# Performance work log

Measured on AMD Instinct MI355X. Metric: run time of the kernel, lower is better.

Reference implementation:

```python
import jax, jax.numpy as jnp
import numpy as np


def setup_inputs() -> dict:
    key = jax.random.key(0)
    k1, k2, k3, k4, k5 = jax.random.split(key, 5)
    N, T, D, H = 256, 64, 1024, 1024
    x = jax.random.normal(k1, (N, T, D), dtype=jnp.float32)
    A = jax.random.normal(k2, (N, H, 4, 4), dtype=jnp.float32)
    Wx = jax.random.normal(k3, (D, 4 * H), dtype=jnp.float32) / np.sqrt(D)
    Wh = jax.random.normal(k4, (H, 4 * H), dtype=jnp.float32) / np.sqrt(H)
    Wattn = jax.random.normal(k5, (H, 4 * H), dtype=jnp.float32) / np.sqrt(H)
    b = jnp.zeros((4 * H,), dtype=jnp.float32)
    return {"x": x, "A": A, "Wx": Wx, "Wh": Wh, "Wattn": Wattn, "b": b}


def reference(x, A, Wx, Wh, Wattn, b):
    N, T, D = x.shape
    H = A.shape[1]
    A_flat = A.reshape(N, H, 16)           # (N, H, 16) flattened 4x4 grid
    scale = 1.0 / jnp.sqrt(jnp.asarray(H, dtype=x.dtype))

    h0 = A.mean(axis=(2, 3))               # (N, H)
    c0 = h0

    def step(carry, xt):
        prev_h, prev_c = carry
        # scaled dot-product attention over the 16 spatial locations
        scores = jnp.einsum('nh,nhl->nl', prev_h, A_flat) * scale  # (N, 16)
        w = jax.nn.softmax(scores, axis=1)
        attn = jnp.einsum('nhl,nl->nh', A_flat, w)                 # (N, H)
        # fused LSTM gate pre-activation
        a = xt @ Wx + prev_h @ Wh + attn @ Wattn + b               # (N, 4H)
        ai, af, ao, ag = jnp.split(a, 4, axis=1)
        i = jax.nn.sigmoid(ai)
        f = jax.nn.sigmoid(af)
        o = jax.nn.sigmoid(ao)
        g = jnp.tanh(ag)
        next_c = f * prev_c + i * g
        next_h = o * jnp.tanh(next_c)
        return (next_h, next_c), next_h

    xs = jnp.swapaxes(x, 0, 1)             # (T, N, D)
    _, hs = jax.lax.scan(step, (h0, c0), xs)
    return jnp.swapaxes(hs, 0, 1)          # (N, T, H)
```

## Files before the change

kernel.cpp:

```cpp
#include <hip/hip_runtime.h>

typedef _Float16 f16;
typedef _Float16 f16x4 __attribute__((ext_vector_type(4)));
typedef _Float16 f16x8 __attribute__((ext_vector_type(8)));
typedef float f32x4 __attribute__((ext_vector_type(4)));

#define N_ 256
#define T_ 64
#define D_ 1024
#define H_ 1024
#define K3 3072
#define G4 4096

__global__ void k_transpose(const float* __restrict__ Wx, const float* __restrict__ Wh,
                            const float* __restrict__ Wattn, f16* __restrict__ W3T) {
    __shared__ float tile[32][33];
    int j0 = blockIdx.x * 32;
    int k0 = blockIdx.y * 32;
    int tx = threadIdx.x;
    int ty = threadIdx.y;
    for (int i = 0; i < 4; i++) {
        int k = k0 + ty + i * 8;
        const float* W = (k < 1024) ? Wx : ((k < 2048) ? Wh : Wattn);
        int kr = k & 1023;
        tile[ty + i * 8][tx] = W[(size_t)kr * 4096 + j0 + tx];
    }
    __syncthreads();
    for (int i = 0; i < 4; i++) {
        int j = j0 + ty + i * 8;
        W3T[(size_t)j * K3 + k0 + tx] = (f16)tile[tx][ty + i * 8];
    }
}

__global__ void k_castA(const float* __restrict__ A, f16* __restrict__ A16) {
    int i = blockIdx.x * 256 + threadIdx.x;
    float4 v = ((const float4*)A)[i];
    f16x4 h4 = {(f16)v.x, (f16)v.y, (f16)v.z, (f16)v.w};
    ((f16x4*)A16)[i] = h4;
}

__global__ void k_castX(const float* __restrict__ x, f16* __restrict__ x16) {
    size_t i = (size_t)blockIdx.x * 2048 + (size_t)threadIdx.x * 8;
    float4 v0 = *(const float4*)(x + i);
    float4 v1 = *(const float4*)(x + i + 4);
    f16x8 h;
    h[0] = (f16)v0.x; h[1] = (f16)v0.y; h[2] = (f16)v0.z; h[3] = (f16)v0.w;
    h[4] = (f16)v1.x; h[5] = (f16)v1.y; h[6] = (f16)v1.z; h[7] = (f16)v1.w;
    *(f16x8*)(x16 + i) = h;
}

__global__ void k_init(const float* __restrict__ A, f16* __restrict__ Zh,
                       float* __restrict__ c, float* __restrict__ spart) {
    int n = blockIdx.x;
    int tid = threadIdx.x;
    __shared__ float sred[256][16];
    float s[16];
#pragma unroll
    for (int l = 0; l < 16; l++) s[l] = 0.f;
    for (int i = 0; i < 4; i++) {
        int h = tid + i * 256;
        const float* Ap = A + (size_t)n * 16384 + h * 16;
        float a[16];
        float sum = 0.f;
#pragma unroll
        for (int l = 0; l < 16; l++) { a[l] = Ap[l]; sum += a[l]; }
        float h0 = sum * (1.f / 16.f);
        c[n * 1024 + h] = h0;
        Zh[n * 1024 + h] = (f16)h0;
#pragma unroll
        for (int l = 0; l < 16; l++) s[l] += h0 * a[l];
    }
#pragma unroll
    for (int l = 0; l < 16; l++) sred[tid][l] = s[l];
    __syncthreads();
    for (int st = 128; st > 0; st >>= 1) {
        if (tid < st) {
#pragma unroll
            for (int l = 0; l < 16; l++) sred[tid][l] += sred[tid + st][l];
        }
        __syncthreads();
    }
    if (tid < 16) spart[(size_t)n * 16 + tid] = sred[0][tid];
    for (int i = 0; i < 4; i++) {
        int idx = tid * 4 + i;
        if (idx < 1008) {
            int ht = 1 + (idx >> 4);
            int l = idx & 15;
            spart[((size_t)ht * 256 + n) * 16 + l] = 0.f;
        }
    }
}

__global__ void k_attn(const float* __restrict__ spart, const f16* __restrict__ A16,
                       f16* __restrict__ Za) {
    int n = blockIdx.x;
    int tid = threadIdx.x;
    __shared__ float sred[16][17];
    __shared__ float sfin[16];
    int g = tid >> 4;
    int l = tid & 15;
    float p = 0.f;
#pragma unroll
    for (int i = 0; i < 4; i++) {
        int ht = g + i * 16;
        p += spart[((size_t)ht * 256 + n) * 16 + l];
    }
    sred[g][l] = p;
    __syncthreads();
    if (tid < 16) {
        float s = 0.f;
#pragma unroll
        for (int gg = 0; gg < 16; gg++) s += sred[gg][tid];
        sfin[tid] = s;
    }
    __syncthreads();
    float w[16];
    float mx = -1e30f;
#pragma unroll
    for (int ll = 0; ll < 16; ll++) { w[ll] = sfin[ll] * 0.03125f; mx = fmaxf(mx, w[ll]); }
    float sum = 0.f;
#pragma unroll
    for (int ll = 0; ll < 16; ll++) { w[ll] = __expf(w[ll] - mx); sum += w[ll]; }
    float inv = 1.f / sum;
#pragma unroll
    for (int ll = 0; ll < 16; ll++) w[ll] *= inv;
    for (int i = 0; i < 4; i++) {
        int h = tid * 4 + i;
        const f16* Ap = A16 + (size_t)n * 16384 + h * 16;
        f16x8 a0 = *(const f16x8*)(Ap);
        f16x8 a1 = *(const f16x8*)(Ap + 8);
        float acc = 0.f;
#pragma unroll
        for (int ll = 0; ll < 8; ll++) acc += (float)a0[ll] * w[ll] + (float)a1[ll] * w[ll + 8];
        Za[n * 1024 + h] = (f16)acc;
    }
}

__global__ __launch_bounds__(512, 2) void k_step(
    const f16* __restrict__ x16, const f16* __restrict__ W3T,
    const f16* __restrict__ Zin, f16* __restrict__ Zout,
    const f16* __restrict__ Za, const f16* __restrict__ A16,
    const float* __restrict__ b, float* __restrict__ c,
    float* __restrict__ spart, float* __restrict__ out, int t) {
    __shared__ float Gs[4][4][64 * 17];
    __shared__ float Hs[64 * 17];

    int tid = threadIdx.x;
    int wave = tid >> 6;
    int lane = tid & 63;
    int m16 = lane & 15;
    int quad = lane >> 4;
    int bid = blockIdx.x;
    int ht = bid & 63;
    int n0 = (bid >> 6) << 6;
    int hc = ht * 16;

    f32x4 acc[4][4];
#pragma unroll
    for (int g = 0; g < 4; g++)
#pragma unroll
        for (int m = 0; m < 4; m++) acc[g][m] = (f32x4){0.f, 0.f, 0.f, 0.f};

    const f16* brow[4];
#pragma unroll
    for (int g = 0; g < 4; g++)
        brow[g] = W3T + (size_t)(g * 1024 + hc + m16) * K3 + quad * 8;

    size_t offx[4], offz[4];
#pragma unroll
    for (int mt = 0; mt < 4; mt++) {
        int n = n0 + mt * 16 + m16;
        offx[mt] = (size_t)n * (T_ * 1024);
        offz[mt] = (size_t)n * 1024;
    }
    const f16* xbase = x16 + (size_t)t * 1024 + quad * 8;
    const f16* zbase0 = Zin + quad * 8;
    const f16* zbase1 = Za + quad * 8;

    int kbase = wave * 384;
#pragma unroll 2
    for (int s = 0; s < 12; s++) {
        int k = kbase + s * 32;
        int seg = k >> 10;
        int kk = k & 1023;
        const f16* base;
        const size_t* off;
        if (seg == 0)      { base = xbase;  off = offx; }
        else if (seg == 1) { base = zbase0; off = offz; }
        else               { base = zbase1; off = offz; }
        f16x8 a[4], bb[4];
#pragma unroll
        for (int mt = 0; mt < 4; mt++) a[mt] = *(const f16x8*)(base + off[mt] + kk);
#pragma unroll
        for (int g = 0; g < 4; g++) bb[g] = *(const f16x8*)(brow[g] + k);
#pragma unroll
        for (int g = 0; g < 4; g++)
#pragma unroll
            for (int mt = 0; mt < 4; mt++)
                acc[g][mt] = __builtin_amdgcn_mfma_f32_16x16x32_f16(a[mt], bb[g], acc[g][mt], 0, 0, 0);
    }

    if (wave < 4) {
#pragma unroll
        for (int g = 0; g < 4; g++)
#pragma unroll
            for (int mt = 0; mt < 4; mt++)
#pragma unroll
                for (int r = 0; r < 4; r++)
                    Gs[wave][g][(mt * 16 + quad * 4 + r) * 17 + m16] = acc[g][mt][r];
    }
    __syncthreads();
    if (wave >= 4) {
        int sl = wave - 4;
#pragma unroll
        for (int g = 0; g < 4; g++)
#pragma unroll
            for (int mt = 0; mt < 4; mt++)
#pragma unroll
                for (int r = 0; r < 4; r++)
                    Gs[sl][g][(mt * 16 + quad * 4 + r) * 17 + m16] += acc[g][mt][r];
    }
    __syncthreads();

    for (int i = 0; i < 2; i++) {
        int idx = i * 512 + tid;
        int nn = idx >> 4;
        int hh = idx & 15;
        int gi = nn * 17 + hh;
        int gn = n0 + nn;
        int gh = hc + hh;
        float ai = Gs[0][0][gi] + Gs[1][0][gi] + Gs[2][0][gi] + Gs[3][0][gi] + b[gh];
        float af = Gs[0][1][gi] + Gs[1][1][gi] + Gs[2][1][gi] + Gs[3][1][gi] + b[1024 + gh];
        float ao = Gs[0][2][gi] + Gs[1][2][gi] + Gs[2][2][gi] + Gs[3][2][gi] + b[2048 + gh];
        float ag = Gs[0][3][gi] + Gs[1][3][gi] + Gs[2][3][gi] + Gs[3][3][gi] + b[3072 + gh];
        float ig = 1.f / (1.f + __expf(-ai));
        float fg = 1.f / (1.f + __expf(-af));
        float og = 1.f / (1.f + __expf(-ao));
        float gg = tanhf(ag);
        float cn = fg * c[gn * 1024 + gh] + ig * gg;
        c[gn * 1024 + gh] = cn;
        float hn = og * tanhf(cn);
        out[((size_t)gn * T_ + t) * 1024 + gh] = hn;
        Zout[gn * 1024 + gh] = (f16)hn;
        Hs[gi] = hn;
    }
    __syncthreads();

    for (int i = 0; i < 2; i++) {
        int idx = i * 512 + tid;
        int nn = idx >> 4;
        int l = idx & 15;
        int gn = n0 + nn;
        const f16* Ap = A16 + (size_t)gn * 16384 + hc * 16 + l;
        float s = 0.f;
#pragma unroll
        for (int hh = 0; hh < 16; hh++)
            s += Hs[nn * 17 + hh] * (float)Ap[hh * 16];
        spart[((size_t)ht * 256 + gn) * 16 + l] = s;
    }
}

extern "C" void kernel_launch(void* const* d_in, const int* in_sizes, int n_in,
                              void* d_out, int out_size, void* d_ws, size_t ws_size,
                              hipStream_t stream) {
    const float* x     = (const float*)d_in[0];
    const float* A     = (const float*)d_in[1];
    const float* Wx    = (const float*)d_in[2];
    const float* Wh    = (const float*)d_in[3];
    const float* Wattn = (const float*)d_in[4];
    const float* b     = (const float*)d_in[5];
    float* out = (float*)d_out;

    char* ws = (char*)d_ws;
    size_t off = 0;
    f16* W3T = (f16*)(ws + off); off += (size_t)G4 * K3 * 2;
    f16* x16 = (f16*)(ws + off); off += (size_t)N_ * T_ * D_ * 2;
    f16* A16 = (f16*)(ws + off); off += (size_t)N_ * H_ * 16 * 2;
    f16* Zh0 = (f16*)(ws + off); off += (size_t)N_ * H_ * 2;
    f16* Zh1 = (f16*)(ws + off); off += (size_t)N_ * H_ * 2;
    f16* Za  = (f16*)(ws + off); off += (size_t)N_ * H_ * 2;
    float* c = (float*)(ws + off); off += (size_t)N_ * H_ * 4;
    float* spart = (float*)(ws + off); off += (size_t)64 * N_ * 16 * 4;

    k_transpose<<<dim3(128, 96), dim3(32, 8), 0, stream>>>(Wx, Wh, Wattn, W3T);
    k_castA<<<4096, 256, 0, stream>>>(A, A16);
    k_castX<<<8192, 256, 0, stream>>>(x, x16);
    k_init<<<256, 256, 0, stream>>>(A, Zh0, c, spart);
    for (int t = 0; t < T_; t++) {
        f16* Zin  = (t & 1) ? Zh1 : Zh0;
        f16* Zout = (t & 1) ? Zh0 : Zh1;
        k_attn<<<256, 256, 0, stream>>>(spart, A16, Za);
        k_step<<<256, 512, 0, stream>>>(x16, W3T, Zin, Zout, Za, A16, b, c, spart, out, t);
    }
}
```

Baseline: 2.240 ms.

## Pack weights, inputs, hidden state and A into MFMA-tile-contiguous layouts

Weights are transposed into per-(h-tile, gate, k-slice) blocks of 16x32 halves, and x, h and the attention context are stored as [k-slice][n][32]. This lets each wave's MFMA operand loads hit contiguous 512-byte chunks instead of strided rows. A is transposed to [n][l][h] so the attention and score kernels use vectorized f16x8 loads, and the h16 write is vectorized. Launch bounds are raised to request 4 blocks per CU, which may increase register pressure or spilling.

```diff
diff --git a/kernel.cpp b/kernel.cpp
--- a/kernel.cpp
+++ b/kernel.cpp
@@ -13,7 +13,7 @@
 #define G4 4096
 
 __global__ void k_transpose(const float* __restrict__ Wx, const float* __restrict__ Wh,
-                            const float* __restrict__ Wattn, f16* __restrict__ W3T) {
+                            const float* __restrict__ Wattn, f16* __restrict__ W3P) {
     __shared__ float tile[32][33];
     int j0 = blockIdx.x * 32;
     int k0 = blockIdx.y * 32;
@@ -28,28 +28,52 @@
     __syncthreads();
     for (int i = 0; i < 4; i++) {
         int j = j0 + ty + i * 8;
-        W3T[(size_t)j * K3 + k0 + tx] = (f16)tile[tx][ty + i * 8];
-    }
-}
-
-__global__ void k_castA(const float* __restrict__ A, f16* __restrict__ A16) {
-    int i = blockIdx.x * 256 + threadIdx.x;
-    float4 v = ((const float4*)A)[i];
-    f16x4 h4 = {(f16)v.x, (f16)v.y, (f16)v.z, (f16)v.w};
-    ((f16x4*)A16)[i] = h4;
-}
-
-__global__ void k_castX(const float* __restrict__ x, f16* __restrict__ x16) {
-    size_t i = (size_t)blockIdx.x * 2048 + (size_t)threadIdx.x * 8;
-    float4 v0 = *(const float4*)(x + i);
-    float4 v1 = *(const float4*)(x + i + 4);
+        int ht = (j & 1023) >> 4;
+        int g = j >> 10;
+        int m16 = j & 15;
+        W3P[(size_t)((ht * 4 + g) * 96 + blockIdx.y) * 512 + m16 * 32 + tx] =
+            (f16)tile[tx][ty + i * 8];
+    }
+}
+
+__global__ void k_packX(const float* __restrict__ x, f16* __restrict__ xp) {
+    int bid = blockIdx.x;
+    int n = bid >> 6;
+    int t = bid & 63;
+    int k = threadIdx.x * 8;
+    const float* src = x + ((size_t)(n * 64 + t)) * 1024 + k;
+    float4 v0 = *(const float4*)src;
+    float4 v1 = *(const float4*)(src + 4);
     f16x8 h;
     h[0] = (f16)v0.x; h[1] = (f16)v0.y; h[2] = (f16)v0.z; h[3] = (f16)v0.w;
     h[4] = (f16)v1.x; h[5] = (f16)v1.y; h[6] = (f16)v1.z; h[7] = (f16)v1.w;
-    *(f16x8*)(x16 + i) = h;
-}
-
-__global__ void k_init(const float* __restrict__ A, f16* __restrict__ Zh,
+    int s = k >> 5, o = k & 31;
+    *(f16x8*)(xp + ((size_t)(t * 32 + s) * 256 + n) * 32 + o) = h;
+}
+
+__global__ void k_packA(const float* __restrict__ A, f16* __restrict__ A16T) {
+    __shared__ f16 tile[256][17];
+    int n = blockIdx.x;
+    int tid = threadIdx.x;
+    for (int c4 = 0; c4 < 4; c4++) {
+        int h = c4 * 256 + tid;
+        const float* Ap = A + (size_t)n * 16384 + h * 16;
+#pragma unroll
+        for (int l = 0; l < 16; l++) tile[tid][l] = (f16)Ap[l];
+        __syncthreads();
+        int l = tid >> 4;
+        int hs = (tid & 15) * 16;
+        f16 v[16];
+#pragma unroll
+        for (int j = 0; j < 16; j++) v[j] = tile[hs + j][l];
+        f16* dst = A16T + (size_t)n * 16384 + l * 1024 + c4 * 256 + hs;
+        *(f16x8*)dst = *(f16x8*)v;
+        *(f16x8*)(dst + 8) = *(f16x8*)(v + 8);
+        __syncthreads();
+    }
+}
+
+__global__ void k_init(const float* __restrict__ A, f16* __restrict__ zp0,
                        float* __restrict__ c, float* __restrict__ spart) {
     int n = blockIdx.x;
     int tid = threadIdx.x;
@@ -66,7 +90,7 @@
         for (int l = 0; l < 16; l++) { a[l] = Ap[l]; sum += a[l]; }
         float h0 = sum * (1.f / 16.f);
         c[n * 1024 + h] = h0;
-        Zh[n * 1024 + h] = (f16)h0;
+        zp0[((size_t)(h >> 5) * 256 + n) * 32 + (h & 31)] = (f16)h0;
 #pragma unroll
         for (int l = 0; l < 16; l++) s[l] += h0 * a[l];
     }
@@ -91,8 +115,8 @@
     }
 }
 
-__global__ void k_attn(const float* __restrict__ spart, const f16* __restrict__ A16,
-                       f16* __restrict__ Za) {
+__global__ void k_attn(const float* __restrict__ spart, const f16* __restrict__ A16T,
+                       f16* __restrict__ zap) {
     int n = blockIdx.x;
     int tid = threadIdx.x;
     __shared__ float sred[16][17];
@@ -101,10 +125,8 @@
     int l = tid & 15;
     float p = 0.f;
 #pragma unroll
-    for (int i = 0; i < 4; i++) {
-        int ht = g + i * 16;
-        p += spart[((size_t)ht * 256 + n) * 16 + l];
-    }
+    for (int i = 0; i < 4; i++)
+        p += spart[((size_t)(g + i * 16) * 256 + n) * 16 + l];
     sred[g][l] = p;
     __syncthreads();
     if (tid < 16) {
@@ -124,22 +146,28 @@
     float inv = 1.f / sum;
 #pragma unroll
     for (int ll = 0; ll < 16; ll++) w[ll] *= inv;
-    for (int i = 0; i < 4; i++) {
-        int h = tid * 4 + i;
-        const f16* Ap = A16 + (size_t)n * 16384 + h * 16;
-        f16x8 a0 = *(const f16x8*)(Ap);
-        f16x8 a1 = *(const f16x8*)(Ap + 8);
-        float acc = 0.f;
-#pragma unroll
-        for (int ll = 0; ll < 8; ll++) acc += (float)a0[ll] * w[ll] + (float)a1[ll] * w[ll + 8];
-        Za[n * 1024 + h] = (f16)acc;
-    }
-}
-
-__global__ __launch_bounds__(512, 2) void k_step(
-    const f16* __restrict__ x16, const f16* __restrict__ W3T,
-    const f16* __restrict__ Zin, f16* __restrict__ Zout,
-    const f16* __restrict__ Za, const f16* __restrict__ A16,
+    if (tid < 128) {
+        int h = tid * 8;
+        float acc[8];
+#pragma unroll
+        for (int e = 0; e < 8; e++) acc[e] = 0.f;
+#pragma unroll
+        for (int ll = 0; ll < 16; ll++) {
+            f16x8 av = *(const f16x8*)(A16T + (size_t)n * 16384 + ll * 1024 + h);
+#pragma unroll
+            for (int e = 0; e < 8; e++) acc[e] += (float)av[e] * w[ll];
+        }
+        f16x8 hv;
+#pragma unroll
+        for (int e = 0; e < 8; e++) hv[e] = (f16)acc[e];
+        *(f16x8*)(zap + ((size_t)(h >> 5) * 256 + n) * 32 + (h & 31)) = hv;
+    }
+}
+
+__global__ __launch_bounds__(512, 4) void k_step(
+    const f16* __restrict__ xp, const f16* __restrict__ W3P,
+    const f16* __restrict__ zin, f16* __restrict__ zout,
+    const f16* __restrict__ zap, const f16* __restrict__ A16T,
     const float* __restrict__ b, float* __restrict__ c,
     float* __restrict__ spart, float* __restrict__ out, int t) {
     __shared__ float Gs[4][4][64 * 17];
@@ -164,35 +192,27 @@
     const f16* brow[4];
 #pragma unroll
     for (int g = 0; g < 4; g++)
-        brow[g] = W3T + (size_t)(g * 1024 + hc + m16) * K3 + quad * 8;
-
-    size_t offx[4], offz[4];
-#pragma unroll
-    for (int mt = 0; mt < 4; mt++) {
-        int n = n0 + mt * 16 + m16;
-        offx[mt] = (size_t)n * (T_ * 1024);
-        offz[mt] = (size_t)n * 1024;
-    }
-    const f16* xbase = x16 + (size_t)t * 1024 + quad * 8;
-    const f16* zbase0 = Zin + quad * 8;
-    const f16* zbase1 = Za + quad * 8;
-
-    int kbase = wave * 384;
+        brow[g] = W3P + (size_t)((ht * 4 + g) * 96) * 512 + m16 * 32 + quad * 8;
+
+    size_t offm[4];
+#pragma unroll
+    for (int mt = 0; mt < 4; mt++)
+        offm[mt] = (size_t)(n0 + mt * 16 + m16) * 32 + quad * 8;
+    const f16* bx = xp + (size_t)t * 262144;
+
+    int sg0 = wave * 12;
 #pragma unroll 2
     for (int s = 0; s < 12; s++) {
-        int k = kbase + s * 32;
-        int seg = k >> 10;
-        int kk = k & 1023;
-        const f16* base;
-        const size_t* off;
-        if (seg == 0)      { base = xbase;  off = offx; }
-        else if (seg == 1) { base = zbase0; off = offz; }
-        else               { base = zbase1; off = offz; }
+        int sg = sg0 + s;
+        int seg = sg >> 5;
+        int sl = sg & 31;
+        const f16* base = (seg == 0) ? bx : ((seg == 1) ? zin : zap);
+        base += (size_t)sl * 8192;
         f16x8 a[4], bb[4];
 #pragma unroll
-        for (int mt = 0; mt < 4; mt++) a[mt] = *(const f16x8*)(base + off[mt] + kk);
-#pragma unroll
-        for (int g = 0; g < 4; g++) bb[g] = *(const f16x8*)(brow[g] + k);
+        for (int mt = 0; mt < 4; mt++) a[mt] = *(const f16x8*)(base + offm[mt]);
+#pragma unroll
+        for (int g = 0; g < 4; g++) bb[g] = *(const f16x8*)(brow[g] + (size_t)sg * 512);
 #pragma unroll
         for (int g = 0; g < 4; g++)
 #pragma unroll
@@ -241,21 +261,32 @@
         c[gn * 1024 + gh] = cn;
         float hn = og * tanhf(cn);
         out[((size_t)gn * T_ + t) * 1024 + gh] = hn;
-        Zout[gn * 1024 + gh] = (f16)hn;
         Hs[gi] = hn;
     }
     __syncthreads();
+
+    if (tid < 128) {
+        int nn = tid >> 1;
+        int h0 = (tid & 1) * 8;
+        f16x8 hv;
+#pragma unroll
+        for (int e = 0; e < 8; e++) hv[e] = (f16)Hs[nn * 17 + h0 + e];
+        int gh = hc + h0;
+        *(f16x8*)(zout + ((size_t)(gh >> 5) * 256 + (n0 + nn)) * 32 + (gh & 31)) = hv;
+    }
 
     for (int i = 0; i < 2; i++) {
         int idx = i * 512 + tid;
         int nn = idx >> 4;
         int l = idx & 15;
         int gn = n0 + nn;
-        const f16* Ap = A16 + (size_t)gn * 16384 + hc * 16 + l;
+        const f16* Ap = A16T + (size_t)gn * 16384 + l * 1024 + hc;
+        f16x8 a0 = *(const f16x8*)Ap;
+        f16x8 a1 = *(const f16x8*)(Ap + 8);
         float s = 0.f;
 #pragma unroll
-        for (int hh = 0; hh < 16; hh++)
-            s += Hs[nn * 17 + hh] * (float)Ap[hh * 16];
+        for (int j = 0; j < 8; j++)
+            s += Hs[nn * 17 + j] * (float)a0[j] + Hs[nn * 17 + 8 + j] * (float)a1[j];
         spart[((size_t)ht * 256 + gn) * 16 + l] = s;
     }
 }
@@ -273,23 +304,23 @@
 
     char* ws = (char*)d_ws;
     size_t off = 0;
-    f16* W3T = (f16*)(ws + off); off += (size_t)G4 * K3 * 2;
-    f16* x16 = (f16*)(ws + off); off += (size_t)N_ * T_ * D_ * 2;
-    f16* A16 = (f16*)(ws + off); off += (size_t)N_ * H_ * 16 * 2;
-    f16* Zh0 = (f16*)(ws + off); off += (size_t)N_ * H_ * 2;
-    f16* Zh1 = (f16*)(ws + off); off += (size_t)N_ * H_ * 2;
-    f16* Za  = (f16*)(ws + off); off += (size_t)N_ * H_ * 2;
-    float* c = (float*)(ws + off); off += (size_t)N_ * H_ * 4;
+    f16* W3P  = (f16*)(ws + off); off += (size_t)G4 * K3 * 2;
+    f16* xp   = (f16*)(ws + off); off += (size_t)N_ * T_ * D_ * 2;
+    f16* A16T = (f16*)(ws + off); off += (size_t)N_ * H_ * 16 * 2;
+    f16* zp0  = (f16*)(ws + off); off += (size_t)N_ * H_ * 2;
+    f16* zp1  = (f16*)(ws + off); off += (size_t)N_ * H_ * 2;
+    f16* zap  = (f16*)(ws + off); off += (size_t)N_ * H_ * 2;
+    float* c  = (float*)(ws + off); off += (size_t)N_ * H_ * 4;
     float* spart = (float*)(ws + off); off += (size_t)64 * N_ * 16 * 4;
 
-    k_transpose<<<dim3(128, 96), dim3(32, 8), 0, stream>>>(Wx, Wh, Wattn, W3T);
-    k_castA<<<4096, 256, 0, stream>>>(A, A16);
-    k_castX<<<8192, 256, 0, stream>>>(x, x16);
-    k_init<<<256, 256, 0, stream>>>(A, Zh0, c, spart);
+    k_transpose<<<dim3(128, 96), dim3(32, 8), 0, stream>>>(Wx, Wh, Wattn, W3P);
+    k_packX<<<16384, 128, 0, stream>>>(x, xp);
+    k_packA<<<256, 256, 0, stream>>>(A, A16T);
+    k_init<<<256, 256, 0, stream>>>(A, zp0, c, spart);
     for (int t = 0; t < T_; t++) {
-        f16* Zin  = (t & 1) ? Zh1 : Zh0;
-        f16* Zout = (t & 1) ? Zh0 : Zh1;
-        k_attn<<<256, 256, 0, stream>>>(spart, A16, Za);
-        k_step<<<256, 512, 0, stream>>>(x16, W3T, Zin, Zout, Za, A16, b, c, spart, out, t);
-    }
-}
+        f16* zin  = (t & 1) ? zp1 : zp0;
+        f16* zout = (t & 1) ? zp0 : zp1;
+        k_attn<<<256, 256, 0, stream>>>(spart, A16T, zap);
+        k_step<<<256, 512, 0, stream>>>(xp, W3P, zin, zout, zap, A16T, b, c, spart, out, t);
+    }
+}
```

New measurement: 2.302 ms. +2.8%, slower.
